# Performance work log

Hardware: AMD Instinct MI355X
Metric: run time of the kernel (lower is better)

Reference implementation:

```python
import jax, jax.numpy as jnp
import numpy as np

N = 50000
E = 800000
DIMS = [(8, 16), (16, 16), (16, 16)]  # (in, out) per layer


def setup_inputs() -> dict:
    key = jax.random.key(0)
    ks = jax.random.split(key, 32)
    inp = {}
    inp['x'] = jax.random.normal(ks[0], (N, 8), dtype=jnp.float32)
    inp['pos'] = jax.random.normal(ks[1], (N, 3), dtype=jnp.float32)
    k = 2
    for i, (ci, co) in enumerate(DIMS):
        d = ci * co
        inp[f'lin_w{i}'] = jax.random.normal(ks[k], (3, d), dtype=jnp.float32); k += 1
        inp[f'lin_b{i}'] = jax.random.normal(ks[k], (d,), dtype=jnp.float32); k += 1
        inp[f'gamma{i}'] = jax.random.normal(ks[k], (d,), dtype=jnp.float32); k += 1
        inp[f'beta{i}'] = jax.random.normal(ks[k], (d,), dtype=jnp.float32); k += 1
        inp[f'root{i}'] = jax.random.normal(ks[k], (ci, co), dtype=jnp.float32); k += 1
        inp[f'bias{i}'] = jax.random.normal(ks[k], (co,), dtype=jnp.float32); k += 1
    inp['batch'] = jnp.zeros((N,), dtype=jnp.int32)
    inp['idx'] = jnp.sort(jax.random.randint(ks[k], (25000,), 0, N, dtype=jnp.int32)); k += 1
    inp['edge_index'] = jax.random.randint(ks[k], (2, E), 0, N, dtype=jnp.int32)
    return inp


def _nnconv(x, pseudo, src, dst, lin_w, lin_b, gamma, beta, root, bias, ci, co):
    # edge MLP (Linear -> batchnorm(eval, affine) -> ReLU), plain_last=False
    w = jax.nn.relu((pseudo @ lin_w + lin_b) * gamma + beta)  # [E, ci*co]
    w = w.reshape(-1, ci, co)                                  # [E, ci, co]
    msg = jnp.einsum('ei,eio->eo', x[src], w)                  # per-edge vec-mat
    s = jax.ops.segment_sum(msg, dst, num_segments=N)          # scatter-sum
    cnt = jax.ops.segment_sum(jnp.ones((msg.shape[0],), x.dtype), dst, num_segments=N)
    aggr = s / jnp.maximum(cnt, 1.0)[:, None]                  # scatter-mean
    return aggr + x @ root + bias


def reference(x, pos, lin_w0, lin_b0, gamma0, beta0, root0, bias0,
              lin_w1, lin_b1, gamma1, beta1, root1, bias1,
              lin_w2, lin_b2, gamma2, beta2, root2, bias2,
              batch, idx, edge_index):
    src, dst = edge_index[0], edge_index[1]
    pseudo = pos[dst] - pos[src]  # patch_size is None
    params = [
        (lin_w0, lin_b0, gamma0, beta0, root0, bias0),
        (lin_w1, lin_b1, gamma1, beta1, root1, bias1),
        (lin_w2, lin_b2, gamma2, beta2, root2, bias2),
    ]
    h = x
    for (ci, co), p in zip(DIMS, params):
        h = jax.nn.relu(_nnconv(h, pseudo, src, dst, *p, ci, co))  # drop_act=False
    return h[idx], pos[idx], batch[idx]
```

## Files before the change

### kernel.cpp

```cpp
#include <hip/hip_runtime.h>

#define N_NODES 50000
#define N_EDGES 800000
#define M_IDX   25000
#define DMAX    64

__global__ __launch_bounds__(256) void prep_kernel(
    const int*   __restrict__ ei,
    const float* __restrict__ pos,
    int*         __restrict__ cnt,
    float4*      __restrict__ pdata,
    int E)
{
    int e = blockIdx.x * blockDim.x + threadIdx.x;
    if (e >= E) return;
    int t = ei[E + e];
    int s = ei[e];
    int p = atomicAdd(&cnt[t], 1);
    float4 pd;
    pd.x = pos[t * 3 + 0] - pos[s * 3 + 0];
    pd.y = pos[t * 3 + 1] - pos[s * 3 + 1];
    pd.z = pos[t * 3 + 2] - pos[s * 3 + 2];
    pd.w = __int_as_float(s);
    if (p < DMAX) pdata[(size_t)t * DMAX + p] = pd;
}

template<int CI>
__global__ __launch_bounds__(256) void node_fused_kernel(
    const float4* __restrict__ pdata,
    const int*    __restrict__ cnt,
    const float*  __restrict__ h_in,
    const float*  __restrict__ lin_w,
    const float*  __restrict__ lin_b,
    const float*  __restrict__ gamma,
    const float*  __restrict__ beta,
    const float*  __restrict__ root,
    const float*  __restrict__ bias,
    float*        __restrict__ h_out,
    int N)
{
    int tid = blockIdx.x * blockDim.x + threadIdx.x;
    if (tid >= N * 16) return;
    const int t = tid >> 4, o = tid & 15;
    const int d = CI * 16;

    float W0[CI], W1[CI], W2[CI], B[CI];
#pragma unroll
    for (int i = 0; i < CI; ++i) {
        int j = i * 16 + o;
        float g = gamma[j];
        W0[i] = lin_w[j] * g;
        W1[i] = lin_w[d + j] * g;
        W2[i] = lin_w[2 * d + j] * g;
        B[i]  = fmaf(lin_b[j], g, beta[j]);
    }

    const int deg = cnt[t];
    const int dl  = min(deg, DMAX);
    const float4* __restrict__ row = pdata + (size_t)t * DMAX;

    float acc = 0.f;
    int p = 0;
    for (; p + 2 <= dl; p += 2) {
        float4 pd0 = row[p];
        float4 pd1 = row[p + 1];
        const float4* xp0 = (const float4*)(h_in + (size_t)__float_as_int(pd0.w) * CI);
        const float4* xp1 = (const float4*)(h_in + (size_t)__float_as_int(pd1.w) * CI);
        float x0[CI], x1[CI];
#pragma unroll
        for (int q = 0; q < CI / 4; ++q) {
            float4 a = xp0[q];
            x0[4 * q + 0] = a.x; x0[4 * q + 1] = a.y;
            x0[4 * q + 2] = a.z; x0[4 * q + 3] = a.w;
            float4 b = xp1[q];
            x1[4 * q + 0] = b.x; x1[4 * q + 1] = b.y;
            x1[4 * q + 2] = b.z; x1[4 * q + 3] = b.w;
        }
#pragma unroll
        for (int i = 0; i < CI; ++i) {
            float w0 = fmaf(pd0.z, W2[i], fmaf(pd0.y, W1[i], fmaf(pd0.x, W0[i], B[i])));
            acc = fmaf(x0[i], fmaxf(w0, 0.f), acc);
            float w1 = fmaf(pd1.z, W2[i], fmaf(pd1.y, W1[i], fmaf(pd1.x, W0[i], B[i])));
            acc = fmaf(x1[i], fmaxf(w1, 0.f), acc);
        }
    }
    if (p < dl) {
        float4 pd0 = row[p];
        const float4* xp0 = (const float4*)(h_in + (size_t)__float_as_int(pd0.w) * CI);
        float x0[CI];
#pragma unroll
        for (int q = 0; q < CI / 4; ++q) {
            float4 a = xp0[q];
            x0[4 * q + 0] = a.x; x0[4 * q + 1] = a.y;
            x0[4 * q + 2] = a.z; x0[4 * q + 3] = a.w;
        }
#pragma unroll
        for (int i = 0; i < CI; ++i) {
            float w0 = fmaf(pd0.z, W2[i], fmaf(pd0.y, W1[i], fmaf(pd0.x, W0[i], B[i])));
            acc = fmaf(x0[i], fmaxf(w0, 0.f), acc);
        }
    }

    float r = fmaf(acc, 1.0f / fmaxf((float)deg, 1.0f), bias[o]);
    const float4* hp = (const float4*)(h_in + (size_t)t * CI);
#pragma unroll
    for (int q = 0; q < CI / 4; ++q) {
        float4 v = hp[q];
        r = fmaf(v.x, root[(4 * q + 0) * 16 + o], r);
        r = fmaf(v.y, root[(4 * q + 1) * 16 + o], r);
        r = fmaf(v.z, root[(4 * q + 2) * 16 + o], r);
        r = fmaf(v.w, root[(4 * q + 3) * 16 + o], r);
    }
    h_out[tid] = fmaxf(r, 0.f);
}

__global__ __launch_bounds__(256) void gather_kernel(
    const float* __restrict__ h,
    const float* __restrict__ pos,
    const int*   __restrict__ batch,
    const int*   __restrict__ idx,
    float*       __restrict__ out,
    int M)
{
    int j = blockIdx.x * blockDim.x + threadIdx.x;
    if (j >= M) return;
    int n = idx[j];
    float4*       o4 = (float4*)out + (size_t)j * 4;
    const float4* h4 = (const float4*)(h + (size_t)n * 16);
    o4[0] = h4[0]; o4[1] = h4[1]; o4[2] = h4[2]; o4[3] = h4[3];
    float* po = out + (size_t)M * 16 + (size_t)j * 3;
    po[0] = pos[n * 3 + 0];
    po[1] = pos[n * 3 + 1];
    po[2] = pos[n * 3 + 2];
    ((int*)out)[(size_t)M * 19 + j] = batch[n];
}

extern "C" void kernel_launch(void* const* d_in, const int* in_sizes, int n_in,
                              void* d_out, int out_size, void* d_ws, size_t ws_size,
                              hipStream_t stream) {
    const float* x      = (const float*)d_in[0];
    const float* pos    = (const float*)d_in[1];
    const float* lin_w0 = (const float*)d_in[2];
    const float* lin_b0 = (const float*)d_in[3];
    const float* gamma0 = (const float*)d_in[4];
    const float* beta0  = (const float*)d_in[5];
    const float* root0  = (const float*)d_in[6];
    const float* bias0  = (const float*)d_in[7];
    const float* lin_w1 = (const float*)d_in[8];
    const float* lin_b1 = (const float*)d_in[9];
    const float* gamma1 = (const float*)d_in[10];
    const float* beta1  = (const float*)d_in[11];
    const float* root1  = (const float*)d_in[12];
    const float* bias1  = (const float*)d_in[13];
    const float* lin_w2 = (const float*)d_in[14];
    const float* lin_b2 = (const float*)d_in[15];
    const float* gamma2 = (const float*)d_in[16];
    const float* beta2  = (const float*)d_in[17];
    const float* root2  = (const float*)d_in[18];
    const float* bias2  = (const float*)d_in[19];
    const int*   batch  = (const int*)d_in[20];
    const int*   idx    = (const int*)d_in[21];
    const int*   ei     = (const int*)d_in[22];
    float*       out    = (float*)d_out;

    float4* pdata = (float4*)d_ws;
    float*  hA    = (float*)(pdata + (size_t)N_NODES * DMAX);
    float*  hB    = hA + (size_t)N_NODES * 16;
    int*    cnt   = (int*)(hB + (size_t)N_NODES * 16);

    hipMemsetAsync(cnt, 0, N_NODES * sizeof(int), stream);
    prep_kernel<<<(N_EDGES + 255) / 256, 256, 0, stream>>>(ei, pos, cnt, pdata, N_EDGES);

    const int NB = (N_NODES * 16 + 255) / 256;

    node_fused_kernel<8><<<NB, 256, 0, stream>>>(pdata, cnt, x,
        lin_w0, lin_b0, gamma0, beta0, root0, bias0, hA, N_NODES);
    node_fused_kernel<16><<<NB, 256, 0, stream>>>(pdata, cnt, hA,
        lin_w1, lin_b1, gamma1, beta1, root1, bias1, hB, N_NODES);
    node_fused_kernel<16><<<NB, 256, 0, stream>>>(pdata, cnt, hB,
        lin_w2, lin_b2, gamma2, beta2, root2, bias2, hA, N_NODES);

    gather_kernel<<<(M_IDX + 255) / 256, 256, 0, stream>>>(hA, pos, batch, idx, out, M_IDX);
}
```

Baseline: 303.8 us.

## Split node edge loop across two half-warps and use packed fp32 FMA

Each node is now handled by 32 lanes instead of 16: two 16-lane halves process alternating edges and combine partial sums with a cross-lane shuffle. The per-edge vec-mat math is rewritten with two-wide float vectors so the compiler can emit packed FMA/max instructions. This shortens the serial per-thread edge loop and raises parallelism. In exchange, per-thread weight setup is duplicated, the grid doubles, and half the lanes idle during the final store.

```diff
diff --git a/kernel.cpp b/kernel.cpp
--- a/kernel.cpp
+++ b/kernel.cpp
@@ -4,6 +4,8 @@
 #define N_EDGES 800000
 #define M_IDX   25000
 #define DMAX    64
+
+typedef float v2f __attribute__((ext_vector_type(2)));
 
 __global__ __launch_bounds__(256) void prep_kernel(
     const int*   __restrict__ ei,
@@ -26,7 +28,37 @@
 }
 
 template<int CI>
-__global__ __launch_bounds__(256) void node_fused_kernel(
+__device__ __forceinline__ void edge_accum(
+    const float4 pd, const float* __restrict__ h_in,
+    const v2f* __restrict__ W0, const v2f* __restrict__ W1,
+    const v2f* __restrict__ W2, const v2f* __restrict__ Bv,
+    v2f& acc)
+{
+    const int s = __float_as_int(pd.w);
+    const float4* xp = (const float4*)(h_in + (size_t)s * CI);
+    v2f xv[CI / 2];
+#pragma unroll
+    for (int q = 0; q < CI / 4; ++q) {
+        float4 a = xp[q];
+        v2f lo; lo.x = a.x; lo.y = a.y;
+        v2f hi; hi.x = a.z; hi.y = a.w;
+        xv[2 * q]     = lo;
+        xv[2 * q + 1] = hi;
+    }
+    v2f px = pd.x, py = pd.y, pz = pd.z;
+    v2f zero = 0.f;
+#pragma unroll
+    for (int q = 0; q < CI / 2; ++q) {
+        v2f w = __builtin_elementwise_fma(pz, W2[q],
+                __builtin_elementwise_fma(py, W1[q],
+                __builtin_elementwise_fma(px, W0[q], Bv[q])));
+        w = __builtin_elementwise_max(w, zero);
+        acc = __builtin_elementwise_fma(xv[q], w, acc);
+    }
+}
+
+template<int CI>
+__global__ __launch_bounds__(256, 2) void node_fused_kernel(
     const float4* __restrict__ pdata,
     const int*    __restrict__ cnt,
     const float*  __restrict__ h_in,
@@ -39,67 +71,45 @@
     float*        __restrict__ h_out,
     int N)
 {
-    int tid = blockIdx.x * blockDim.x + threadIdx.x;
-    if (tid >= N * 16) return;
-    const int t = tid >> 4, o = tid & 15;
-    const int d = CI * 16;
+    int gid = blockIdx.x * blockDim.x + threadIdx.x;
+    if (gid >= N * 32) return;
+    const int t    = gid >> 5;
+    const int half = (gid >> 4) & 1;
+    const int o    = gid & 15;
+    const int d    = CI * 16;
 
-    float W0[CI], W1[CI], W2[CI], B[CI];
+    v2f W0[CI / 2], W1[CI / 2], W2[CI / 2], Bv[CI / 2];
 #pragma unroll
-    for (int i = 0; i < CI; ++i) {
-        int j = i * 16 + o;
-        float g = gamma[j];
-        W0[i] = lin_w[j] * g;
-        W1[i] = lin_w[d + j] * g;
-        W2[i] = lin_w[2 * d + j] * g;
-        B[i]  = fmaf(lin_b[j], g, beta[j]);
+    for (int q = 0; q < CI / 2; ++q) {
+#pragma unroll
+        for (int u = 0; u < 2; ++u) {
+            int j = (2 * q + u) * 16 + o;
+            float g = gamma[j];
+            W0[q][u] = lin_w[j] * g;
+            W1[q][u] = lin_w[d + j] * g;
+            W2[q][u] = lin_w[2 * d + j] * g;
+            Bv[q][u] = fmaf(lin_b[j], g, beta[j]);
+        }
     }
 
     const int deg = cnt[t];
     const int dl  = min(deg, DMAX);
     const float4* __restrict__ row = pdata + (size_t)t * DMAX;
 
-    float acc = 0.f;
-    int p = 0;
-    for (; p + 2 <= dl; p += 2) {
+    v2f acc0 = 0.f, acc1 = 0.f;
+    int p = half;
+    for (; p + 2 < dl; p += 4) {
         float4 pd0 = row[p];
-        float4 pd1 = row[p + 1];
-        const float4* xp0 = (const float4*)(h_in + (size_t)__float_as_int(pd0.w) * CI);
-        const float4* xp1 = (const float4*)(h_in + (size_t)__float_as_int(pd1.w) * CI);
-        float x0[CI], x1[CI];
-#pragma unroll
-        for (int q = 0; q < CI / 4; ++q) {
-            float4 a = xp0[q];
-            x0[4 * q + 0] = a.x; x0[4 * q + 1] = a.y;
-            x0[4 * q + 2] = a.z; x0[4 * q + 3] = a.w;
-            float4 b = xp1[q];
-            x1[4 * q + 0] = b.x; x1[4 * q + 1] = b.y;
-            x1[4 * q + 2] = b.z; x1[4 * q + 3] = b.w;
-        }
-#pragma unroll
-        for (int i = 0; i < CI; ++i) {
-            float w0 = fmaf(pd0.z, W2[i], fmaf(pd0.y, W1[i], fmaf(pd0.x, W0[i], B[i])));
-            acc = fmaf(x0[i], fmaxf(w0, 0.f), acc);
-            float w1 = fmaf(pd1.z, W2[i], fmaf(pd1.y, W1[i], fmaf(pd1.x, W0[i], B[i])));
-            acc = fmaf(x1[i], fmaxf(w1, 0.f), acc);
-        }
+        float4 pd1 = row[p + 2];
+        edge_accum<CI>(pd0, h_in, W0, W1, W2, Bv, acc0);
+        edge_accum<CI>(pd1, h_in, W0, W1, W2, Bv, acc1);
     }
     if (p < dl) {
         float4 pd0 = row[p];
-        const float4* xp0 = (const float4*)(h_in + (size_t)__float_as_int(pd0.w) * CI);
-        float x0[CI];
-#pragma unroll
-        for (int q = 0; q < CI / 4; ++q) {
-            float4 a = xp0[q];
-            x0[4 * q + 0] = a.x; x0[4 * q + 1] = a.y;
-            x0[4 * q + 2] = a.z; x0[4 * q + 3] = a.w;
-        }
-#pragma unroll
-        for (int i = 0; i < CI; ++i) {
-            float w0 = fmaf(pd0.z, W2[i], fmaf(pd0.y, W1[i], fmaf(pd0.x, W0[i], B[i])));
-            acc = fmaf(x0[i], fmaxf(w0, 0.f), acc);
-        }
+        edge_accum<CI>(pd0, h_in, W0, W1, W2, Bv, acc0);
     }
+    float acc = acc0.x + acc0.y + acc1.x + acc1.y;
+    acc += __shfl_xor(acc, 16);
 
     float r = fmaf(acc, 1.0f / fmaxf((float)deg, 1.0f), bias[o]);
     const float4* hp = (const float4*)(h_in + (size_t)t * CI);
@@ -111,7 +121,7 @@
         r = fmaf(v.z, root[(4 * q + 2) * 16 + o], r);
         r = fmaf(v.w, root[(4 * q + 3) * 16 + o], r);
     }
-    h_out[tid] = fmaxf(r, 0.f);
+    if (half == 0) h_out[t * 16 + o] = fmaxf(r, 0.f);
 }
 
 __global__ __launch_bounds__(256) void gather_kernel(
@@ -171,7 +181,7 @@
     hipMemsetAsync(cnt, 0, N_NODES * sizeof(int), stream);
     prep_kernel<<<(N_EDGES + 255) / 256, 256, 0, stream>>>(ei, pos, cnt, pdata, N_EDGES);
 
-    const int NB = (N_NODES * 16 + 255) / 256;
+    const int NB = (N_NODES * 32 + 255) / 256;
 
     node_fused_kernel<8><<<NB, 256, 0, stream>>>(pdata, cnt, x,
         lin_w0, lin_b0, gamma0, beta0, root0, bias0, hA, N_NODES);
```

After: 379.0 us. +24.8%, slower.

## Assign one wavefront per node with four edge groups and cache edge weights in LDS

Applied to the files above, without the earlier changes.

The node kernel now maps a full 64-lane wavefront to each destination node. Four groups of 16 lanes each handle a strided subset of the incoming edges, and their partial sums are combined with xor shuffles. The folded Linear/batchnorm weights move from per-thread registers into a shared float4 table, which lowers register pressure and spreads each node's edge list across more lanes, but adds LDS reads and a block barrier. The prep kernel also processes two edges per thread so that more loads and atomics are in flight at once.

```diff
diff --git a/kernel.cpp b/kernel.cpp
--- a/kernel.cpp
+++ b/kernel.cpp
@@ -12,21 +12,35 @@
     float4*      __restrict__ pdata,
     int E)
 {
-    int e = blockIdx.x * blockDim.x + threadIdx.x;
-    if (e >= E) return;
-    int t = ei[E + e];
-    int s = ei[e];
-    int p = atomicAdd(&cnt[t], 1);
-    float4 pd;
-    pd.x = pos[t * 3 + 0] - pos[s * 3 + 0];
-    pd.y = pos[t * 3 + 1] - pos[s * 3 + 1];
-    pd.z = pos[t * 3 + 2] - pos[s * 3 + 2];
-    pd.w = __int_as_float(s);
-    if (p < DMAX) pdata[(size_t)t * DMAX + p] = pd;
+    const int e0 = blockIdx.x * 512 + threadIdx.x;
+    const int e1 = e0 + 256;
+    const bool v0 = e0 < E, v1 = e1 < E;
+    int t0 = 0, s0 = 0, t1 = 0, s1 = 0;
+    if (v0) { t0 = ei[E + e0]; s0 = ei[e0]; }
+    if (v1) { t1 = ei[E + e1]; s1 = ei[e1]; }
+    int p0 = 0, p1 = 0;
+    if (v0) p0 = atomicAdd(&cnt[t0], 1);
+    if (v1) p1 = atomicAdd(&cnt[t1], 1);
+    if (v0) {
+        float4 pd;
+        pd.x = pos[t0 * 3 + 0] - pos[s0 * 3 + 0];
+        pd.y = pos[t0 * 3 + 1] - pos[s0 * 3 + 1];
+        pd.z = pos[t0 * 3 + 2] - pos[s0 * 3 + 2];
+        pd.w = __int_as_float(s0);
+        if (p0 < DMAX) pdata[(size_t)t0 * DMAX + p0] = pd;
+    }
+    if (v1) {
+        float4 pd;
+        pd.x = pos[t1 * 3 + 0] - pos[s1 * 3 + 0];
+        pd.y = pos[t1 * 3 + 1] - pos[s1 * 3 + 1];
+        pd.z = pos[t1 * 3 + 2] - pos[s1 * 3 + 2];
+        pd.w = __int_as_float(s1);
+        if (p1 < DMAX) pdata[(size_t)t1 * DMAX + p1] = pd;
+    }
 }
 
 template<int CI>
-__global__ __launch_bounds__(256) void node_fused_kernel(
+__global__ __launch_bounds__(256) void node_wave_kernel(
     const float4* __restrict__ pdata,
     const int*    __restrict__ cnt,
     const float*  __restrict__ h_in,
@@ -39,67 +53,61 @@
     float*        __restrict__ h_out,
     int N)
 {
-    int tid = blockIdx.x * blockDim.x + threadIdx.x;
-    if (tid >= N * 16) return;
-    const int t = tid >> 4, o = tid & 15;
-    const int d = CI * 16;
+    __shared__ float4 wlds[CI * 16];
 
-    float W0[CI], W1[CI], W2[CI], B[CI];
-#pragma unroll
-    for (int i = 0; i < CI; ++i) {
-        int j = i * 16 + o;
-        float g = gamma[j];
-        W0[i] = lin_w[j] * g;
-        W1[i] = lin_w[d + j] * g;
-        W2[i] = lin_w[2 * d + j] * g;
-        B[i]  = fmaf(lin_b[j], g, beta[j]);
+    const int tid = threadIdx.x;
+    if (tid < CI * 16) {
+        const int j = tid;
+        const float g = gamma[j];
+        float4 w4;
+        w4.x = lin_w[j] * g;
+        w4.y = lin_w[CI * 16 + j] * g;
+        w4.z = lin_w[2 * CI * 16 + j] * g;
+        w4.w = fmaf(lin_b[j], g, beta[j]);
+        wlds[j] = w4;
     }
+    __syncthreads();
+
+    const int lane = tid & 63;
+    const int eg   = lane >> 4;
+    const int o    = lane & 15;
+    const int t    = blockIdx.x * 4 + (tid >> 6);
 
     const int deg = cnt[t];
     const int dl  = min(deg, DMAX);
     const float4* __restrict__ row = pdata + (size_t)t * DMAX;
 
     float acc = 0.f;
-    int p = 0;
-    for (; p + 2 <= dl; p += 2) {
-        float4 pd0 = row[p];
-        float4 pd1 = row[p + 1];
-        const float4* xp0 = (const float4*)(h_in + (size_t)__float_as_int(pd0.w) * CI);
-        const float4* xp1 = (const float4*)(h_in + (size_t)__float_as_int(pd1.w) * CI);
-        float x0[CI], x1[CI];
+    for (int p = eg; p < dl; p += 8) {
+        const int  p1 = p + 4;
+        const bool v1 = p1 < dl;
+        float4 pdA = row[p];
+        float4 pdB = v1 ? row[p1] : pdA;
+        const float4* xa = (const float4*)(h_in + (size_t)__float_as_int(pdA.w) * CI);
+        const float4* xb = (const float4*)(h_in + (size_t)__float_as_int(pdB.w) * CI);
+        float xA[CI], xB[CI];
 #pragma unroll
         for (int q = 0; q < CI / 4; ++q) {
-            float4 a = xp0[q];
-            x0[4 * q + 0] = a.x; x0[4 * q + 1] = a.y;
-            x0[4 * q + 2] = a.z; x0[4 * q + 3] = a.w;
-            float4 b = xp1[q];
-            x1[4 * q + 0] = b.x; x1[4 * q + 1] = b.y;
-            x1[4 * q + 2] = b.z; x1[4 * q + 3] = b.w;
+            float4 a = xa[q];
+            xA[4 * q + 0] = a.x; xA[4 * q + 1] = a.y;
+            xA[4 * q + 2] = a.z; xA[4 * q + 3] = a.w;
+            float4 b = xb[q];
+            xB[4 * q + 0] = b.x; xB[4 * q + 1] = b.y;
+            xB[4 * q + 2] = b.z; xB[4 * q + 3] = b.w;
         }
+        float eA = 0.f, eB = 0.f;
 #pragma unroll
         for (int i = 0; i < CI; ++i) {
-            float w0 = fmaf(pd0.z, W2[i], fmaf(pd0.y, W1[i], fmaf(pd0.x, W0[i], B[i])));
-            acc = fmaf(x0[i], fmaxf(w0, 0.f), acc);
-            float w1 = fmaf(pd1.z, W2[i], fmaf(pd1.y, W1[i], fmaf(pd1.x, W0[i], B[i])));
-            acc = fmaf(x1[i], fmaxf(w1, 0.f), acc);
+            float4 w4 = wlds[i * 16 + o];
+            float wA = fmaf(pdA.z, w4.z, fmaf(pdA.y, w4.y, fmaf(pdA.x, w4.x, w4.w)));
+            eA = fmaf(xA[i], fmaxf(wA, 0.f), eA);
+            float wB = fmaf(pdB.z, w4.z, fmaf(pdB.y, w4.y, fmaf(pdB.x, w4.x, w4.w)));
+            eB = fmaf(xB[i], fmaxf(wB, 0.f), eB);
         }
+        acc += eA + (v1 ? eB : 0.f);
     }
-    if (p < dl) {
-        float4 pd0 = row[p];
-        const float4* xp0 = (const float4*)(h_in + (size_t)__float_as_int(pd0.w) * CI);
-        float x0[CI];
-#pragma unroll
-        for (int q = 0; q < CI / 4; ++q) {
-            float4 a = xp0[q];
-            x0[4 * q + 0] = a.x; x0[4 * q + 1] = a.y;
-            x0[4 * q + 2] = a.z; x0[4 * q + 3] = a.w;
-        }
-#pragma unroll
-        for (int i = 0; i < CI; ++i) {
-            float w0 = fmaf(pd0.z, W2[i], fmaf(pd0.y, W1[i], fmaf(pd0.x, W0[i], B[i])));
-            acc = fmaf(x0[i], fmaxf(w0, 0.f), acc);
-        }
-    }
+    acc += __shfl_xor(acc, 16);
+    acc += __shfl_xor(acc, 32);
 
     float r = fmaf(acc, 1.0f / fmaxf((float)deg, 1.0f), bias[o]);
     const float4* hp = (const float4*)(h_in + (size_t)t * CI);
@@ -111,7 +119,7 @@
         r = fmaf(v.z, root[(4 * q + 2) * 16 + o], r);
         r = fmaf(v.w, root[(4 * q + 3) * 16 + o], r);
     }
-    h_out[tid] = fmaxf(r, 0.f);
+    if (eg == 0) h_out[t * 16 + o] = fmaxf(r, 0.f);
 }
 
 __global__ __launch_bounds__(256) void gather_kernel(
@@ -169,15 +177,15 @@
     int*    cnt   = (int*)(hB + (size_t)N_NODES * 16);
 
     hipMemsetAsync(cnt, 0, N_NODES * sizeof(int), stream);
-    prep_kernel<<<(N_EDGES + 255) / 256, 256, 0, stream>>>(ei, pos, cnt, pdata, N_EDGES);
+    prep_kernel<<<(N_EDGES + 511) / 512, 256, 0, stream>>>(ei, pos, cnt, pdata, N_EDGES);
 
-    const int NB = (N_NODES * 16 + 255) / 256;
+    const int NB = N_NODES / 4;
 
-    node_fused_kernel<8><<<NB, 256, 0, stream>>>(pdata, cnt, x,
+    node_wave_kernel<8><<<NB, 256, 0, stream>>>(pdata, cnt, x,
         lin_w0, lin_b0, gamma0, beta0, root0, bias0, hA, N_NODES);
-    node_fused_kernel<16><<<NB, 256, 0, stream>>>(pdata, cnt, hA,
+    node_wave_kernel<16><<<NB, 256, 0, stream>>>(pdata, cnt, hA,
         lin_w1, lin_b1, gamma1, beta1, root1, bias1, hB, N_NODES);
-    node_fused_kernel<16><<<NB, 256, 0, stream>>>(pdata, cnt, hB,
+    node_wave_kernel<16><<<NB, 256, 0, stream>>>(pdata, cnt, hB,
         lin_w2, lin_b2, gamma2, beta2, root2, bias2, hA, N_NODES);
 
     gather_kernel<<<(M_IDX + 255) / 256, 256, 0, stream>>>(hA, pos, batch, idx, out, M_IDX);
```

Result: slower. 350.5 us (+15.4%).
